# Optimization experiments

Hardware: AMD Instinct MI355X
Metric: run time of the kernel (lower is better)

Reference implementation:

```python
import jax, jax.numpy as jnp
import numpy as np
import math

NHEADS = 4


def _mab(Q, K, qw, qb, kw, kb, vw, vb, ow, ob, mask):
    """MAB2 from tripletformer: multi-head attention (head split via cat(split,0)),
    softmax scale uses sqrt(FULL dim_V), masked_fill(mask==0, -1e10), residual on
    the projected Q, then O + relu(fc_o(O))."""
    dv = qw.shape[1]
    dh = dv // NHEADS
    B, Nq, _ = Q.shape
    Nk = K.shape[1]
    Qh = (Q @ qw + qb).reshape(B, Nq, NHEADS, dh).transpose(0, 2, 1, 3)  # B,h,Nq,dh
    Kh = (K @ kw + kb).reshape(B, Nk, NHEADS, dh).transpose(0, 2, 1, 3)
    Vh = (K @ vw + vb).reshape(B, Nk, NHEADS, dh).transpose(0, 2, 1, 3)
    att = jnp.einsum('bhqd,bhkd->bhqk', Qh, Kh) * (1.0 / math.sqrt(dv))
    att = jnp.where(mask, att, jnp.asarray(-1e10, att.dtype))
    A = jax.nn.softmax(att, axis=-1)
    Oh = Qh + jnp.einsum('bhqk,bhkd->bhqd', A, Vh)
    O = Oh.transpose(0, 2, 1, 3).reshape(B, Nq, dv)
    return O + jax.nn.relu(O @ ow + ob)


def _forward(context_x, value, mask, obs_len, iff_w, iff_b, ind_points,
             q0w, q0b, k0w, k0b, v0w, v0b, o0w, o0b,
             q1w, q1b, k1w, k1b, v1w, v1b, o1w, o1b):
    B, L = context_x.shape
    D = value.shape[-1]
    mflat = mask.reshape(B, L * D)
    # stable stream compaction: observed entries first, original (time-major,
    # channel-minor) order preserved; truncate to static obs_len
    order = jnp.argsort(-mflat, axis=-1, stable=True)[:, :obs_len]  # (B, N)
    T = jnp.broadcast_to(context_x[:, :, None], (B, L, D)).reshape(B, L * D)
    C = jnp.broadcast_to(jnp.arange(D, dtype=jnp.int32), (B, L, D)).reshape(B, L * D)
    U = value.reshape(B, L * D)
    take = lambda a: jnp.take_along_axis(a, order, axis=-1)
    T_, U_, mk_ = take(T), take(U), take(mflat)
    Ch = jax.nn.one_hot(take(C), D, dtype=value.dtype)  # one_hot(num_classes=dim-2)
    X = jnp.concatenate([Ch, T_[..., None], U_[..., None]], axis=-1) * mk_[..., None]
    Y = jax.nn.relu(X @ iff_w + iff_b) * mk_[..., None]
    key_valid = mk_ > 0                        # (B, N)
    mask1 = key_valid[:, None, None, :]        # mab0: mask padded keys
    mask2 = key_valid[:, None, :, None]        # mab1: mask padded query rows
    Z = Y
    n_layers = ind_points.shape[0]
    for i in range(n_layers):
        I = jnp.broadcast_to(ind_points[i], (B,) + ind_points[i].shape)
        H = _mab(I, Z, q0w[i], q0b[i], k0w[i], k0b[i], v0w[i], v0b[i], o0w[i], o0b[i], mask1)
        Zn = _mab(Z, H, q1w[i], q1b[i], k1w[i], k1b[i], v1w[i], v1b[i], o1w[i], o1b[i], mask2)
        Z = Zn * mk_[..., None] + Z
    return Z, mk_[..., None]


def setup_inputs() -> dict:
    B, L, D, OBS, DK, M, NL = 16, 512, 41, 4096, 128, 128, 3
    key = jax.random.key(0)
    ks = jax.random.split(key, 16)
    context_x = jnp.sort(jax.random.uniform(ks[0], (B, L), dtype=jnp.float32), axis=-1)
    value = jax.random.normal(ks[1], (B, L, D), dtype=jnp.float32)
    # exactly OBS observed entries per batch row -> static packed length
    r = jax.random.uniform(ks[2], (B, L * D))
    kth = jnp.sort(r, axis=-1)[:, OBS]
    mask = (r < kth[:, None]).astype(jnp.float32).reshape(B, L, D)

    def w(k, shape, fan):
        return jax.random.normal(k, shape, dtype=jnp.float32) / math.sqrt(fan)

    inp = dict(
        context_x=context_x, value=value, mask=mask, obs_len=OBS,
        iff_w=w(ks[3], (D + 2, DK), D + 2), iff_b=jnp.zeros((DK,), jnp.float32),
        ind_points=w(ks[4], (NL, M, DK), DK),
    )
    for j, n in enumerate(['q0', 'k0', 'v0', 'o0', 'q1', 'k1', 'v1', 'o1']):
        inp[n + 'w'] = w(ks[5 + j], (NL, DK, DK), DK)
        inp[n + 'b'] = jnp.zeros((NL, DK), jnp.float32)
    return inp


def reference(context_x, value, mask, obs_len, iff_w, iff_b, ind_points,
              q0w, q0b, k0w, k0b, v0w, v0b, o0w, o0b,
              q1w, q1b, k1w, k1b, v1w, v1b, o1w, o1b):
    return _forward(context_x, value, mask, obs_len, iff_w, iff_b, ind_points,
                    q0w, q0b, k0w, k0b, v0w, v0b, o0w, o0b,
                    q1w, q1b, k1w, k1b, v1w, v1b, o1w, o1b)
```

## Files before the change

kernel.cpp:

```cpp
#include <hip/hip_runtime.h>
#include <math.h>

#define NBATCH 16
#define SEQL   512
#define DIM    41
#define LDFLAT (SEQL*DIM)
#define OBS    4096
#define DK     128
#define NH     4
#define DH     32

typedef short bf16x8 __attribute__((ext_vector_type(8)));
typedef short short8v __attribute__((ext_vector_type(8)));
typedef float floatx4 __attribute__((ext_vector_type(4)));

__device__ __forceinline__ short f2bf(float f) {
  union { float f; unsigned u; } v;
  v.f = f;
  unsigned r = (v.u + 0x7fffu + ((v.u >> 16) & 1u)) >> 16;
  return (short)r;
}
__device__ __forceinline__ float bf2f(short s) {
  union { unsigned u; float f; } v;
  v.u = ((unsigned)(unsigned short)s) << 16;
  return v.f;
}

__device__ __forceinline__ void stage_w(short* Wl, const short* __restrict__ Wt,
                                        int tid) {
#pragma unroll
  for (int i = tid * 8; i < 128 * 128; i += 2048)
    *(int4*)&Wl[(i >> 7) * 136 + (i & 127)] = *(const int4*)&Wt[i];
}
__device__ __forceinline__ void load_af(const short* Xl, int wv, int lm,
                                        int quad, bf16x8 af[4]) {
#pragma unroll
  for (int kc = 0; kc < 4; kc++)
    af[kc] = *(bf16x8*)&Xl[(wv * 16 + lm) * 136 + kc * 32 + quad * 8];
}
__device__ __forceinline__ void gemm8(const short* Wl, const bf16x8 af[4],
                                      int lm, int quad, floatx4 acc[8]) {
#pragma unroll
  for (int nt = 0; nt < 8; nt++) acc[nt] = (floatx4){0.f, 0.f, 0.f, 0.f};
#pragma unroll
  for (int kc = 0; kc < 4; kc++) {
    bf16x8 a = af[kc];
#pragma unroll
    for (int nt = 0; nt < 8; nt++) {
      bf16x8 b = *(bf16x8*)&Wl[(nt * 16 + lm) * 136 + kc * 32 + quad * 8];
      acc[nt] = __builtin_amdgcn_mfma_f32_16x16x32_bf16(a, b, acc[nt], 0, 0, 0);
    }
  }
}
__device__ __forceinline__ void store_sl(short* Sl, const floatx4 acc[8],
                                         const float* __restrict__ bias,
                                         int wv, int lm, int quad) {
#pragma unroll
  for (int nt = 0; nt < 8; nt++) {
    int col = nt * 16 + lm;
    float bn = bias[col];
#pragma unroll
    for (int r = 0; r < 4; r++)
      Sl[(wv * 16 + quad * 4 + r) * 136 + col] = f2bf(acc[nt][r] + bn);
  }
}
__device__ __forceinline__ void write_hs(const short* Sl,
                                         short* __restrict__ out, int rb,
                                         int nshift, int tid) {
  int rr = tid >> 2, hh = tid & 3;
  int r = rb + rr;
  int bb = r >> nshift, nn = r & ((1 << nshift) - 1);
  size_t o = (((size_t)(bb * NH + hh) << nshift) + nn) * 32;
#pragma unroll
  for (int j = 0; j < 4; j++)
    *(int4*)&out[o + j * 8] = *(int4*)&Sl[rr * 136 + hh * 32 + j * 8];
}

__global__ __launch_bounds__(1024) void prep_build_kernel(
    const float* __restrict__ q0w, const float* __restrict__ k0w,
    const float* __restrict__ v0w, const float* __restrict__ o0w,
    const float* __restrict__ q1w, const float* __restrict__ k1w,
    const float* __restrict__ v1w, const float* __restrict__ o1w,
    short* __restrict__ Wt,
    const float* __restrict__ mask, int* __restrict__ order,
    float* __restrict__ mk_out, float* __restrict__ mk_out2) {
  __shared__ float Tl[128 * 132];
  __shared__ int wsums[16];
  __shared__ int s_total_ones;
  __shared__ int s_chunk_ones;
  __shared__ int s_ones_base;
  __shared__ int s_zeros_base;
  int tid = threadIdx.x;

  if (blockIdx.x < 24) {
    int id = blockIdx.x, l = id >> 3, wi = id & 7;
    const float* s;
    switch (wi) {
      case 0: s = q0w; break; case 1: s = k0w; break;
      case 2: s = v0w; break; case 3: s = o0w; break;
      case 4: s = q1w; break; case 5: s = k1w; break;
      case 6: s = v1w; break; default: s = o1w; break;
    }
    s += (size_t)l * 16384;
    for (int i = tid * 4; i < 16384; i += 4096) {
      int k = i >> 7, n = i & 127;
      float4 x = *(const float4*)&s[i];
      Tl[k * 132 + n + 0] = x.x; Tl[k * 132 + n + 1] = x.y;
      Tl[k * 132 + n + 2] = x.z; Tl[k * 132 + n + 3] = x.w;
    }
    __syncthreads();
    short* dst = Wt + (size_t)id * 16384;
    int n = tid >> 3, k0 = (tid & 7) * 16;
    for (int jc = 0; jc < 2; jc++) {
      short8v t;
#pragma unroll
      for (int j = 0; j < 8; j++) t[j] = f2bf(Tl[(k0 + jc * 8 + j) * 132 + n]);
      *(short8v*)&dst[n * 128 + k0 + jc * 8] = t;
    }
    return;
  }

  int b = blockIdx.x - 24;
  const float* m = mask + (size_t)b * LDFLAT;
  int lane = tid & 63, w = tid >> 6;

  int cnt = 0;
  for (int j = tid; j < LDFLAT; j += 1024) cnt += (m[j] > 0.f) ? 1 : 0;
  for (int off = 32; off > 0; off >>= 1) cnt += __shfl_xor(cnt, off);
  if (lane == 0) wsums[w] = cnt;
  __syncthreads();
  if (tid == 0) {
    int t = 0;
    for (int i = 0; i < 16; i++) t += wsums[i];
    s_total_ones = t; s_ones_base = 0; s_zeros_base = 0;
  }
  __syncthreads();
  int total_ones = s_total_ones;

  for (int c0 = 0; c0 < LDFLAT; c0 += 1024) {
    __syncthreads();
    int j = c0 + tid;
    bool valid = (j < LDFLAT);
    float mv = valid ? m[j] : 0.f;
    int one = (valid && mv > 0.f) ? 1 : 0;
    int v = one;
    for (int off = 1; off < 64; off <<= 1) {
      int t = __shfl_up(v, (unsigned)off);
      if (lane >= off) v += t;
    }
    if (lane == 63) wsums[w] = v;
    __syncthreads();
    if (tid == 0) {
      int run = 0;
      for (int i = 0; i < 16; i++) { int t = wsums[i]; wsums[i] = run; run += t; }
      s_chunk_ones = run;
    }
    __syncthreads();
    int ones_before = (v - one) + wsums[w];
    int ob = s_ones_base, zb = s_zeros_base, chunk_ones = s_chunk_ones;
    int rem = LDFLAT - c0;
    int chunk_valid = rem < 1024 ? rem : 1024;
    int valid_before = tid < rem ? tid : rem;
    if (valid) {
      int pos = one ? (ob + ones_before)
                    : (total_ones + zb + (valid_before - ones_before));
      if (pos < OBS) {
        order[b * OBS + pos] = j;
        mk_out[b * OBS + pos] = mv;
        mk_out2[b * OBS + pos] = mv;
      }
    }
    __syncthreads();
    if (tid == 0) {
      s_ones_base = ob + chunk_ones;
      s_zeros_base = zb + (chunk_valid - chunk_ones);
    }
  }
}

__global__ __launch_bounds__(256) void fusedA_kernel(
    const int* __restrict__ order, const float* __restrict__ mk_g,
    const float* __restrict__ cx, const float* __restrict__ value,
    const float* __restrict__ iff_w, const float* __restrict__ iff_b,
    float* __restrict__ Z,
    const short* __restrict__ Wk, const float* __restrict__ kbias,
    short* __restrict__ Kb,
    const short* __restrict__ Wv, const float* __restrict__ vbias,
    short* __restrict__ Vb,
    const short* __restrict__ Wq, const float* __restrict__ qbias,
    short* __restrict__ Qb,
    const float* __restrict__ indp, const short* __restrict__ WtAll,
    const float* __restrict__ q0b_all, short* __restrict__ qh_b) {
  __shared__ __align__(16) short Xl[64 * 136];
  __shared__ __align__(16) short Wl[128 * 136];
  __shared__ int   rdd[64];
  __shared__ float rdt[64], rdu[64], rdm[64];
  int tid = threadIdx.x;
  int wv = tid >> 6, lane = tid & 63, lm = lane & 15, quad = lane >> 4;

  if (blockIdx.x >= 1024) {
    int id = blockIdx.x - 1024;
    int l = id >> 1, rbq = (id & 1) * 64;
    const float* X = indp + (size_t)l * 16384 + (size_t)rbq * 128;
    const short* W = WtAll + (size_t)(l * 8) * 16384;
    const float* bias = q0b_all + (size_t)l * 128;
    short* out = qh_b + (size_t)l * 16384;
    for (int i = tid * 4; i < 64 * 128; i += 1024) {
      int rr = i >> 7, c = i & 127;
      float4 x = *(const float4*)&X[i];
      *(short4*)&Xl[rr * 136 + c] =
          make_short4(f2bf(x.x), f2bf(x.y), f2bf(x.z), f2bf(x.w));
    }
    stage_w(Wl, W, tid);
    __syncthreads();
    bf16x8 af[4];
    load_af(Xl, wv, lm, quad, af);
    floatx4 acc[8];
    gemm8(Wl, af, lm, quad, acc);
    store_sl(Xl, acc, bias, wv, lm, quad);
    write_hs(Xl, out, rbq, 7, tid);
    return;
  }

  int rb = blockIdx.x * 64;
  if (tid < 64) {
    int idx = rb + tid;
    int b = idx >> 12;
    int j = order[idx];
    int l = j / DIM;
    rdd[tid] = j - l * DIM;
    rdt[tid] = cx[b * SEQL + l];
    rdu[tid] = value[(size_t)b * LDFLAT + j];
    rdm[tid] = mk_g[idx];
  }
  stage_w(Wl, Wk, tid);
  __syncthreads();
  for (int i = tid * 4; i < 64 * 128; i += 1024) {
    int rr = i >> 7, k = i & 127;
    float4 w0 = *(const float4*)&iff_w[rdd[rr] * DK + k];
    float4 w1 = *(const float4*)&iff_w[41 * DK + k];
    float4 w2 = *(const float4*)&iff_w[42 * DK + k];
    float4 b4 = *(const float4*)&iff_b[k];
    float t = rdt[rr], u = rdu[rr], mkv = rdm[rr];
    float4 z;
    z.x = fmaxf(w0.x + t * w1.x + u * w2.x + b4.x, 0.f) * mkv;
    z.y = fmaxf(w0.y + t * w1.y + u * w2.y + b4.y, 0.f) * mkv;
    z.z = fmaxf(w0.z + t * w1.z + u * w2.z + b4.z, 0.f) * mkv;
    z.w = fmaxf(w0.w + t * w1.w + u * w2.w + b4.w, 0.f) * mkv;
    *(float4*)&Z[(size_t)(rb + rr) * DK + k] = z;
    *(short4*)&Xl[rr * 136 + k] =
        make_short4(f2bf(z.x), f2bf(z.y), f2bf(z.z), f2bf(z.w));
  }
  __syncthreads();
  bf16x8 af[4];
  load_af(Xl, wv, lm, quad, af);
  floatx4 acc[8];
  gemm8(Wl, af, lm, quad, acc);
  store_sl(Xl, acc, kbias, wv, lm, quad);
  write_hs(Xl, Kb, rb, 12, tid);
  __syncthreads();
  stage_w(Wl, Wv, tid);
  __syncthreads();
  gemm8(Wl, af, lm, quad, acc);
  store_sl(Xl, acc, vbias, wv, lm, quad);
  write_hs(Xl, Vb, rb, 12, tid);
  __syncthreads();
  stage_w(Wl, Wq, tid);
  __syncthreads();
  gemm8(Wl, af, lm, quad, acc);
  store_sl(Xl, acc, qbias, wv, lm, quad);
  write_hs(Xl, Qb, rb, 12, tid);
}

__global__ __launch_bounds__(256) void attn1_kernel(
    const short* __restrict__ Qh,
    const short* __restrict__ Kh, const short* __restrict__ Vh,
    const float* __restrict__ mk,
    float* __restrict__ Opart, float* __restrict__ mpart,
    float* __restrict__ lpart) {
  __shared__ __align__(16) short Ql[128 * 40];
  __shared__ __align__(16) short Kc[64 * 40];
  __shared__ __align__(16) short Vtc[32 * 72];
  __shared__ __align__(16) short Pl[128 * 72];
  __shared__ float mkc[64];
  int bh = blockIdx.x;
  int b = bh >> 2, h = bh & 3;
  int ks = blockIdx.y;
  int tid = threadIdx.x;
  int wv = tid >> 6, lane = tid & 63, lm = lane & 15, quad = lane >> 4;

  const short* qbg = Qh + (size_t)h * 128 * 32;
  for (int i = tid * 8; i < 128 * 32; i += 2048) {
    int r = i >> 5, c = i & 31;
    *(int4*)&Ql[r * 40 + c] = *(const int4*)&qbg[i];
  }
  __syncthreads();
  bf16x8 aq[2];
  aq[0] = *(bf16x8*)&Ql[(wv * 32 + lm) * 40 + quad * 8];
  aq[1] = *(bf16x8*)&Ql[(wv * 32 + 16 + lm) * 40 + quad * 8];

  float m_i[2][4], l_i[2][4];
  floatx4 oacc[2][2];
#pragma unroll
  for (int mt = 0; mt < 2; mt++) {
#pragma unroll
    for (int r = 0; r < 4; r++) { m_i[mt][r] = -1e30f; l_i[mt][r] = 0.f; }
    oacc[mt][0] = (floatx4){0.f, 0.f, 0.f, 0.f};
    oacc[mt][1] = (floatx4){0.f, 0.f, 0.f, 0.f};
  }
  const float scale = 0.08838834764831845f;
  const short* kbase = Kh + ((size_t)bh * OBS + ks * 512) * 32;
  const short* vbase = Vh + ((size_t)bh * OBS + ks * 512) * 32;
  const float* mkb = mk + (size_t)b * OBS + ks * 512;

  for (int ch = 0; ch < 8; ch++) {
    __syncthreads();
    {
      int i = tid * 8;
      int r = i >> 5, c = i & 31;
      *(int4*)&Kc[r * 40 + c] = *(const int4*)&kbase[ch * 2048 + i];
      int4 vv4 = *(const int4*)&vbase[ch * 2048 + i];
      short* vv = (short*)&vv4;
#pragma unroll
      for (int j = 0; j < 8; j++) Vtc[(c + j) * 72 + r] = vv[j];
    }
    if (tid < 64) mkc[tid] = mkb[ch * 64 + tid];
    __syncthreads();

    floatx4 sf[2][4];
#pragma unroll
    for (int nt = 0; nt < 4; nt++) {
      bf16x8 bfrag = *(bf16x8*)&Kc[(nt * 16 + lm) * 40 + quad * 8];
      floatx4 z = {0.f, 0.f, 0.f, 0.f};
      sf[0][nt] = __builtin_amdgcn_mfma_f32_16x16x32_bf16(aq[0], bfrag, z, 0, 0, 0);
      sf[1][nt] = __builtin_amdgcn_mfma_f32_16x16x32_bf16(aq[1], bfrag, z, 0, 0, 0);
    }
#pragma unroll
    for (int nt = 0; nt < 4; nt++) {
      float mkv = mkc[nt * 16 + lm];
      bool ok = mkv > 0.f;
#pragma unroll
      for (int mt = 0; mt < 2; mt++)
#pragma unroll
        for (int r = 0; r < 4; r++)
          sf[mt][nt][r] = ok ? sf[mt][nt][r] * scale : -1e10f;
    }
#pragma unroll
    for (int mt = 0; mt < 2; mt++) {
#pragma unroll
      for (int r = 0; r < 4; r++) {
        float mx = fmaxf(fmaxf(sf[mt][0][r], sf[mt][1][r]),
                         fmaxf(sf[mt][2][r], sf[mt][3][r]));
        mx = fmaxf(mx, __shfl_xor(mx, 1));
        mx = fmaxf(mx, __shfl_xor(mx, 2));
        mx = fmaxf(mx, __shfl_xor(mx, 4));
        mx = fmaxf(mx, __shfl_xor(mx, 8));
        float mn = fmaxf(m_i[mt][r], mx);
        float al = __expf(m_i[mt][r] - mn);
        float ps = 0.f;
#pragma unroll
        for (int nt = 0; nt < 4; nt++) {
          float p = __expf(sf[mt][nt][r] - mn);
          sf[mt][nt][r] = p;
          ps += p;
        }
        ps += __shfl_xor(ps, 1);
        ps += __shfl_xor(ps, 2);
        ps += __shfl_xor(ps, 4);
        ps += __shfl_xor(ps, 8);
        l_i[mt][r] = l_i[mt][r] * al + ps;
        m_i[mt][r] = mn;
        oacc[mt][0] *= al;
        oacc[mt][1] *= al;
      }
    }
#pragma unroll
    for (int mt = 0; mt < 2; mt++)
#pragma unroll
      for (int nt = 0; nt < 4; nt++)
#pragma unroll
        for (int r = 0; r < 4; r++)
          Pl[(wv * 32 + mt * 16 + quad * 4 + r) * 72 + nt * 16 + lm] =
              f2bf(sf[mt][nt][r]);
#pragma unroll
    for (int kc = 0; kc < 2; kc++) {
      bf16x8 vf0 = *(bf16x8*)&Vtc[lm * 72 + kc * 32 + quad * 8];
      bf16x8 vf1 = *(bf16x8*)&Vtc[(16 + lm) * 72 + kc * 32 + quad * 8];
#pragma unroll
      for (int mt = 0; mt < 2; mt++) {
        bf16x8 pf = *(bf16x8*)&Pl[(wv * 32 + mt * 16 + lm) * 72 + kc * 32 + quad * 8];
        oacc[mt][0] = __builtin_amdgcn_mfma_f32_16x16x32_bf16(pf, vf0, oacc[mt][0], 0, 0, 0);
        oacc[mt][1] = __builtin_amdgcn_mfma_f32_16x16x32_bf16(pf, vf1, oacc[mt][1], 0, 0, 0);
      }
    }
  }
  float* ob = Opart + (size_t)(ks * 64 + bh) * 128 * 32;
#pragma unroll
  for (int mt = 0; mt < 2; mt++) {
#pragma unroll
    for (int r = 0; r < 4; r++) {
      int row = wv * 32 + mt * 16 + quad * 4 + r;
      ob[(size_t)row * 32 + lm] = oacc[mt][0][r];
      ob[(size_t)row * 32 + 16 + lm] = oacc[mt][1][r];
      if (lm == 0) {
        mpart[(size_t)(ks * 64 + bh) * 128 + row] = m_i[mt][r];
        lpart[(size_t)(ks * 64 + bh) * 128 + row] = l_i[mt][r];
      }
    }
  }
}

__global__ __launch_bounds__(256) void fusedB_kernel(
    const float* __restrict__ Opart, const float* __restrict__ mpart,
    const float* __restrict__ lpart, const short* __restrict__ qh,
    const short* __restrict__ Wo, const float* __restrict__ obias,
    const short* __restrict__ Wk, const float* __restrict__ kbias,
    const short* __restrict__ Wv, const float* __restrict__ vbias,
    short* __restrict__ khb, short* __restrict__ vhb) {
  __shared__ __align__(16) short Xl[64 * 136];
  __shared__ __align__(16) short Wl[128 * 136];
  int tid = threadIdx.x;
  int rb = blockIdx.x * 64;
  int b = rb >> 7, n0 = rb & 127;
  {
    int rr = tid >> 2, hh = tid & 3;
    int n = n0 + rr;
    int bh = b * 4 + hh;
    float mv[8], lv[8], m = -1e30f;
#pragma unroll
    for (int s = 0; s < 8; s++) {
      mv[s] = mpart[(size_t)(s * 64 + bh) * 128 + n];
      lv[s] = lpart[(size_t)(s * 64 + bh) * 128 + n];
      m = fmaxf(m, mv[s]);
    }
    float l = 0.f;
    float oa[32];
#pragma unroll
    for (int d = 0; d < 32; d++) oa[d] = 0.f;
#pragma unroll
    for (int s = 0; s < 8; s++) {
      float w = __expf(mv[s] - m);
      l += lv[s] * w;
      const float* op = &Opart[((size_t)(s * 64 + bh) * 128 + n) * 32];
#pragma unroll
      for (int d4 = 0; d4 < 8; d4++) {
        float4 v = *(const float4*)&op[d4 * 4];
        oa[d4 * 4 + 0] += v.x * w; oa[d4 * 4 + 1] += v.y * w;
        oa[d4 * 4 + 2] += v.z * w; oa[d4 * 4 + 3] += v.w * w;
      }
    }
    float li = 1.f / l;
    const short* qp = &qh[((size_t)hh * 128 + n) * 32];
#pragma unroll
    for (int d = 0; d < 32; d++)
      Xl[rr * 136 + hh * 32 + d] = f2bf(bf2f(qp[d]) + oa[d] * li);
  }
  stage_w(Wl, Wo, tid);
  __syncthreads();
  int wv = tid >> 6, lane = tid & 63, lm = lane & 15, quad = lane >> 4;
  bf16x8 af[4];
  load_af(Xl, wv, lm, quad, af);
  floatx4 acc[8];
  gemm8(Wl, af, lm, quad, acc);
#pragma unroll
  for (int nt = 0; nt < 8; nt++) {
    int col = nt * 16 + lm;
    float bn = obias[col];
#pragma unroll
    for (int r = 0; r < 4; r++) {
      int row = wv * 16 + quad * 4 + r;
      float ov = bf2f(Xl[row * 136 + col]);
      Xl[row * 136 + col] = f2bf(ov + fmaxf(acc[nt][r] + bn, 0.f));
    }
  }
  load_af(Xl, wv, lm, quad, af);
  __syncthreads();
  stage_w(Wl, Wk, tid);
  __syncthreads();
  gemm8(Wl, af, lm, quad, acc);
  store_sl(Xl, acc, kbias, wv, lm, quad);
  write_hs(Xl, khb, rb, 7, tid);
  __syncthreads();
  stage_w(Wl, Wv, tid);
  __syncthreads();
  gemm8(Wl, af, lm, quad, acc);
  store_sl(Xl, acc, vbias, wv, lm, quad);
  write_hs(Xl, vhb, rb, 7, tid);
}

__global__ __launch_bounds__(256) void attn2_kernel(
    const short* __restrict__ Qh, const short* __restrict__ Kh,
    const short* __restrict__ Vh, short* __restrict__ O) {
  __shared__ __align__(16) short Kl[128 * 40];
  __shared__ __align__(16) short Vt[32 * 136];
  __shared__ __align__(16) short Ql[64 * 40];
  __shared__ __align__(16) short Pl[64 * 136];
  int bh = blockIdx.x;
  int b = bh >> 2, h = bh & 3;
  int q0 = blockIdx.y * 64;
  int tid = threadIdx.x;
  int wv = tid >> 6, lane = tid & 63, lm = lane & 15, quad = lane >> 4;
  const short* kb = Kh + (size_t)bh * 128 * 32;
  const short* vb = Vh + (size_t)bh * 128 * 32;
  const short* qb = Qh + ((size_t)bh * OBS + q0) * 32;

  for (int i = tid * 8; i < 128 * 32; i += 2048) {
    int r = i >> 5, c = i & 31;
    *(int4*)&Kl[r * 40 + c] = *(const int4*)&kb[i];
  }
  for (int i = tid * 8; i < 64 * 32; i += 2048) {
    int r = i >> 5, c = i & 31;
    *(int4*)&Ql[r * 40 + c] = *(const int4*)&qb[i];
  }
  for (int i = tid * 8; i < 128 * 32; i += 2048) {
    int r = i >> 5, c = i & 31;
    int4 vv4 = *(const int4*)&vb[i];
    short* vv = (short*)&vv4;
#pragma unroll
    for (int j = 0; j < 8; j++) Vt[(c + j) * 136 + r] = vv[j];
  }
  __syncthreads();

  const float scale = 0.08838834764831845f;
  bf16x8 afrag = *(bf16x8*)&Ql[(wv * 16 + lm) * 40 + quad * 8];
  floatx4 sf[8];
#pragma unroll
  for (int nt = 0; nt < 8; nt++) {
    bf16x8 bfrag = *(bf16x8*)&Kl[(nt * 16 + lm) * 40 + quad * 8];
    floatx4 z = {0.f, 0.f, 0.f, 0.f};
    sf[nt] = __builtin_amdgcn_mfma_f32_16x16x32_bf16(afrag, bfrag, z, 0, 0, 0);
  }
#pragma unroll
  for (int nt = 0; nt < 8; nt++) sf[nt] *= scale;
  float linv[4];
#pragma unroll
  for (int r = 0; r < 4; r++) {
    float mx = sf[0][r];
#pragma unroll
    for (int nt = 1; nt < 8; nt++) mx = fmaxf(mx, sf[nt][r]);
    mx = fmaxf(mx, __shfl_xor(mx, 1));
    mx = fmaxf(mx, __shfl_xor(mx, 2));
    mx = fmaxf(mx, __shfl_xor(mx, 4));
    mx = fmaxf(mx, __shfl_xor(mx, 8));
    float sum = 0.f;
#pragma unroll
    for (int nt = 0; nt < 8; nt++) {
      float p = __expf(sf[nt][r] - mx);
      sf[nt][r] = p;
      sum += p;
    }
    sum += __shfl_xor(sum, 1);
    sum += __shfl_xor(sum, 2);
    sum += __shfl_xor(sum, 4);
    sum += __shfl_xor(sum, 8);
    linv[r] = 1.f / sum;
  }
#pragma unroll
  for (int nt = 0; nt < 8; nt++)
#pragma unroll
    for (int r = 0; r < 4; r++)
      Pl[(wv * 16 + quad * 4 + r) * 136 + nt * 16 + lm] = f2bf(sf[nt][r]);

  floatx4 oacc[2] = {{0.f, 0.f, 0.f, 0.f}, {0.f, 0.f, 0.f, 0.f}};
#pragma unroll
  for (int kc = 0; kc < 4; kc++) {
    bf16x8 pf = *(bf16x8*)&Pl[(wv * 16 + lm) * 136 + kc * 32 + quad * 8];
#pragma unroll
    for (int nt2 = 0; nt2 < 2; nt2++) {
      bf16x8 vf = *(bf16x8*)&Vt[(nt2 * 16 + lm) * 136 + kc * 32 + quad * 8];
      oacc[nt2] = __builtin_amdgcn_mfma_f32_16x16x32_bf16(pf, vf, oacc[nt2], 0, 0, 0);
    }
  }
  short* Ol = Pl;
#pragma unroll
  for (int nt2 = 0; nt2 < 2; nt2++) {
#pragma unroll
    for (int r = 0; r < 4; r++) {
      int qrow = wv * 16 + quad * 4 + r;
      float q = bf2f(Ql[qrow * 40 + nt2 * 16 + lm]);
      Ol[qrow * 136 + nt2 * 16 + lm] = f2bf(q + oacc[nt2][r] * linv[r]);
    }
  }
  int rr = tid >> 2, seg = tid & 3;
  size_t o = ((size_t)b * OBS + q0 + rr) * 128 + h * 32 + seg * 8;
  *(int4*)&O[o] = *(int4*)&Ol[rr * 136 + seg * 8];
}

__global__ __launch_bounds__(256) void fusedC_kernel(
    const short* __restrict__ Ob, const short* __restrict__ Wo,
    const float* __restrict__ obias, const float* __restrict__ mk,
    const float* __restrict__ Zin, float* __restrict__ Zout,
    const short* __restrict__ Wk, const float* __restrict__ kbias,
    short* __restrict__ Kb,
    const short* __restrict__ Wv, const float* __restrict__ vbias,
    short* __restrict__ Vb,
    const short* __restrict__ Wq, const float* __restrict__ qbias,
    short* __restrict__ Qb) {
  __shared__ __align__(16) short Xl[64 * 136];
  __shared__ __align__(16) short Wl[128 * 136];
  int tid = threadIdx.x;
  int rb = blockIdx.x * 64;
  int wv = tid >> 6, lane = tid & 63, lm = lane & 15, quad = lane >> 4;
  for (int i = tid * 8; i < 64 * 128; i += 2048) {
    int rr = i >> 7, c = i & 127;
    *(int4*)&Xl[rr * 136 + c] = *(const int4*)&Ob[(size_t)(rb + rr) * 136 - (size_t)(rb + rr) * 8 + c];
  }
  stage_w(Wl, Wo, tid);
  __syncthreads();
  bf16x8 af[4];
  load_af(Xl, wv, lm, quad, af);
  floatx4 acc[8];
  gemm8(Wl, af, lm, quad, acc);
  __syncthreads();
  float* Fl = (float*)Wl;
#pragma unroll
  for (int nt = 0; nt < 8; nt++) {
    int col = nt * 16 + lm;
    float bn = obias[col];
#pragma unroll
    for (int r = 0; r < 4; r++) {
      int row = wv * 16 + quad * 4 + r;
      int gr = rb + row;
      float ov = bf2f(Xl[row * 136 + col]);
      float f = ov + fmaxf(acc[nt][r] + bn, 0.f);
      Fl[row * 132 + col] = Zin[(size_t)gr * 128 + col] + f * mk[gr];
    }
  }
  {
    int rr = tid >> 2, seg = tid & 3;
    int gr = rb + rr;
#pragma unroll
    for (int j = 0; j < 8; j++) {
      float4 f = *(float4*)&Fl[rr * 132 + seg * 32 + j * 4];
      *(float4*)&Zout[(size_t)gr * 128 + seg * 32 + j * 4] = f;
      if (Wk)
        *(short4*)&Xl[rr * 136 + seg * 32 + j * 4] =
            make_short4(f2bf(f.x), f2bf(f.y), f2bf(f.z), f2bf(f.w));
    }
  }
  if (Wk == nullptr) return;
  load_af(Xl, wv, lm, quad, af);
  __syncthreads();
  stage_w(Wl, Wk, tid);
  __syncthreads();
  gemm8(Wl, af, lm, quad, acc);
  store_sl(Xl, acc, kbias, wv, lm, quad);
  write_hs(Xl, Kb, rb, 12, tid);
  __syncthreads();
  stage_w(Wl, Wv, tid);
  __syncthreads();
  gemm8(Wl, af, lm, quad, acc);
  store_sl(Xl, acc, vbias, wv, lm, quad);
  write_hs(Xl, Vb, rb, 12, tid);
  __syncthreads();
  stage_w(Wl, Wq, tid);
  __syncthreads();
  gemm8(Wl, af, lm, quad, acc);
  store_sl(Xl, acc, qbias, wv, lm, quad);
  write_hs(Xl, Qb, rb, 12, tid);
}

extern "C" void kernel_launch(void* const* d_in, const int* in_sizes, int n_in,
                              void* d_out, int out_size, void* d_ws,
                              size_t ws_size, hipStream_t stream) {
  const float* cx    = (const float*)d_in[0];
  const float* value = (const float*)d_in[1];
  const float* mask  = (const float*)d_in[2];
  const float* iff_w = (const float*)d_in[4];
  const float* iff_b = (const float*)d_in[5];
  const float* indp  = (const float*)d_in[6];
  const float* q0w = (const float*)d_in[7];  const float* q0b = (const float*)d_in[8];
  const float* k0w = (const float*)d_in[9];  const float* k0b = (const float*)d_in[10];
  const float* v0w = (const float*)d_in[11]; const float* v0b = (const float*)d_in[12];
  const float* o0w = (const float*)d_in[13]; const float* o0b = (const float*)d_in[14];
  const float* q1w = (const float*)d_in[15]; const float* q1b = (const float*)d_in[16];
  const float* k1w = (const float*)d_in[17]; const float* k1b = (const float*)d_in[18];
  const float* v1w = (const float*)d_in[19]; const float* v1b = (const float*)d_in[20];
  const float* o1w = (const float*)d_in[21]; const float* o1b = (const float*)d_in[22];

  char* ws = (char*)d_ws;
  short* Wt    = (short*)ws;  ws += (size_t)24 * 16384 * 2;
  int*   order = (int*)ws;    ws += (size_t)NBATCH * OBS * 4;
  float* mk_g  = (float*)ws;  ws += (size_t)NBATCH * OBS * 4;
  float* Z     = (float*)ws;  ws += (size_t)NBATCH * OBS * DK * 4;
  short* Qb    = (short*)ws;  ws += (size_t)NBATCH * OBS * DK * 2;
  short* Kb    = (short*)ws;  ws += (size_t)NBATCH * OBS * DK * 2;
  short* Vb    = (short*)ws;  ws += (size_t)NBATCH * OBS * DK * 2;
  short* Ob    = (short*)ws;  ws += (size_t)NBATCH * OBS * DK * 2;
  short* qh_b  = (short*)ws;  ws += (size_t)3 * 128 * DK * 2;
  short* khb   = (short*)ws;  ws += (size_t)NBATCH * NH * 128 * DH * 2;
  short* vhb   = (short*)ws;  ws += (size_t)NBATCH * NH * 128 * DH * 2;
  float* Opart = (float*)ws;  ws += (size_t)8 * 64 * 128 * 32 * 4;
  float* mpart = (float*)ws;  ws += (size_t)8 * 64 * 128 * 4;
  float* lpart = (float*)ws;  ws += (size_t)8 * 64 * 128 * 4;

  float* outZ  = (float*)d_out;
  float* outMk = outZ + (size_t)NBATCH * OBS * DK;

  prep_build_kernel<<<40, 1024, 0, stream>>>(q0w, k0w, v0w, o0w, q1w, k1w,
                                             v1w, o1w, Wt, mask, order, mk_g,
                                             outMk);

  const short* W[3][8];
  for (int l = 0; l < 3; l++)
    for (int wi = 0; wi < 8; wi++) W[l][wi] = Wt + (size_t)(l * 8 + wi) * 16384;

  fusedA_kernel<<<1030, 256, 0, stream>>>(
      order, mk_g, cx, value, iff_w, iff_b, Z,
      W[0][1], k0b, Kb, W[0][2], v0b, Vb, W[0][4], q1b, Qb,
      indp, Wt, q0b, qh_b);

  for (int l = 0; l < 3; l++) {
    attn1_kernel<<<dim3(64, 8), 256, 0, stream>>>(
        qh_b + (size_t)l * 16384, Kb, Vb, mk_g, Opart, mpart, lpart);
    fusedB_kernel<<<32, 256, 0, stream>>>(
        Opart, mpart, lpart, qh_b + (size_t)l * 16384,
        W[l][3], o0b + (size_t)l * 128,
        W[l][5], k1b + (size_t)l * 128,
        W[l][6], v1b + (size_t)l * 128, khb, vhb);
    attn2_kernel<<<dim3(64, 64), 256, 0, stream>>>(Qb, khb, vhb, Ob);
    if (l < 2) {
      fusedC_kernel<<<1024, 256, 0, stream>>>(
          Ob, W[l][7], o1b + (size_t)l * 128, mk_g, Z, Z,
          W[l + 1][1], k0b + (size_t)(l + 1) * 128, Kb,
          W[l + 1][2], v0b + (size_t)(l + 1) * 128, Vb,
          W[l + 1][4], q1b + (size_t)(l + 1) * 128, Qb);
    } else {
      fusedC_kernel<<<1024, 256, 0, stream>>>(
          Ob, W[l][7], o1b + (size_t)l * 128, mk_g, Z, outZ,
          nullptr, nullptr, nullptr, nullptr, nullptr, nullptr,
          nullptr, nullptr, nullptr);
    }
  }
}
```

Baseline: 513.2 us.

## Read GEMM weight fragments directly from global memory instead of staging in LDS

The fused projection kernels (A, B, C) no longer copy each 128x128 bf16 weight matrix into a shared-memory tile before the MFMA loop. Each lane now loads its B-fragment straight from global memory, which relies on L1/L2 caching of the small weight matrices. This removes the weight LDS buffer and most block-wide barriers, and launch bounds now ask for four blocks per CU to raise occupancy. Per-row input staging is also reorganised so each wave fills only the rows it later reads. The trade-off is strided, partly uncoalesced global fragment loads in place of LDS reads, and some removed barriers may now let waves overwrite the shared scratch tile while other waves still read it.

```diff
diff --git a/kernel.cpp b/kernel.cpp
--- a/kernel.cpp
+++ b/kernel.cpp
@@ -26,31 +26,27 @@
   return v.f;
 }
 
-__device__ __forceinline__ void stage_w(short* Wl, const short* __restrict__ Wt,
-                                        int tid) {
-#pragma unroll
-  for (int i = tid * 8; i < 128 * 128; i += 2048)
-    *(int4*)&Wl[(i >> 7) * 136 + (i & 127)] = *(const int4*)&Wt[i];
+
+__device__ __forceinline__ void gemm8_g(const short* __restrict__ Wg,
+                                        const bf16x8 af[4], int lm, int quad,
+                                        floatx4 acc[8]) {
+#pragma unroll
+  for (int nt = 0; nt < 8; nt++) acc[nt] = (floatx4){0.f, 0.f, 0.f, 0.f};
+#pragma unroll
+  for (int kc = 0; kc < 4; kc++) {
+    bf16x8 a = af[kc];
+#pragma unroll
+    for (int nt = 0; nt < 8; nt++) {
+      bf16x8 b = *(const bf16x8*)&Wg[(size_t)(nt * 16 + lm) * 128 + kc * 32 + quad * 8];
+      acc[nt] = __builtin_amdgcn_mfma_f32_16x16x32_bf16(a, b, acc[nt], 0, 0, 0);
+    }
+  }
 }
 __device__ __forceinline__ void load_af(const short* Xl, int wv, int lm,
                                         int quad, bf16x8 af[4]) {
 #pragma unroll
   for (int kc = 0; kc < 4; kc++)
     af[kc] = *(bf16x8*)&Xl[(wv * 16 + lm) * 136 + kc * 32 + quad * 8];
-}
-__device__ __forceinline__ void gemm8(const short* Wl, const bf16x8 af[4],
-                                      int lm, int quad, floatx4 acc[8]) {
-#pragma unroll
-  for (int nt = 0; nt < 8; nt++) acc[nt] = (floatx4){0.f, 0.f, 0.f, 0.f};
-#pragma unroll
-  for (int kc = 0; kc < 4; kc++) {
-    bf16x8 a = af[kc];
-#pragma unroll
-    for (int nt = 0; nt < 8; nt++) {
-      bf16x8 b = *(bf16x8*)&Wl[(nt * 16 + lm) * 136 + kc * 32 + quad * 8];
-      acc[nt] = __builtin_amdgcn_mfma_f32_16x16x32_bf16(a, b, acc[nt], 0, 0, 0);
-    }
-  }
 }
 __device__ __forceinline__ void store_sl(short* Sl, const floatx4 acc[8],
                                          const float* __restrict__ bias,
@@ -178,7 +174,7 @@
   }
 }
 
-__global__ __launch_bounds__(256) void fusedA_kernel(
+__global__ __launch_bounds__(256, 4) void fusedA_kernel(
     const int* __restrict__ order, const float* __restrict__ mk_g,
     const float* __restrict__ cx, const float* __restrict__ value,
     const float* __restrict__ iff_w, const float* __restrict__ iff_b,
@@ -192,11 +188,10 @@
     const float* __restrict__ indp, const short* __restrict__ WtAll,
     const float* __restrict__ q0b_all, short* __restrict__ qh_b) {
   __shared__ __align__(16) short Xl[64 * 136];
-  __shared__ __align__(16) short Wl[128 * 136];
-  __shared__ int   rdd[64];
-  __shared__ float rdt[64], rdu[64], rdm[64];
   int tid = threadIdx.x;
   int wv = tid >> 6, lane = tid & 63, lm = lane & 15, quad = lane >> 4;
+  int r_l = lane >> 2, seg = lane & 3;
+  int lrow = wv * 16 + r_l;
 
   if (blockIdx.x >= 1024) {
     int id = blockIdx.x - 1024;
@@ -205,69 +200,57 @@
     const short* W = WtAll + (size_t)(l * 8) * 16384;
     const float* bias = q0b_all + (size_t)l * 128;
     short* out = qh_b + (size_t)l * 16384;
-    for (int i = tid * 4; i < 64 * 128; i += 1024) {
-      int rr = i >> 7, c = i & 127;
-      float4 x = *(const float4*)&X[i];
-      *(short4*)&Xl[rr * 136 + c] =
+    const float* Xr = X + (size_t)lrow * 128;
+#pragma unroll
+    for (int jj = 0; jj < 8; jj++) {
+      int col = seg * 32 + jj * 4;
+      float4 x = *(const float4*)&Xr[col];
+      *(short4*)&Xl[lrow * 136 + col] =
           make_short4(f2bf(x.x), f2bf(x.y), f2bf(x.z), f2bf(x.w));
     }
-    stage_w(Wl, W, tid);
-    __syncthreads();
     bf16x8 af[4];
     load_af(Xl, wv, lm, quad, af);
     floatx4 acc[8];
-    gemm8(Wl, af, lm, quad, acc);
+    gemm8_g(W, af, lm, quad, acc);
     store_sl(Xl, acc, bias, wv, lm, quad);
     write_hs(Xl, out, rbq, 7, tid);
     return;
   }
 
   int rb = blockIdx.x * 64;
-  if (tid < 64) {
-    int idx = rb + tid;
-    int b = idx >> 12;
-    int j = order[idx];
-    int l = j / DIM;
-    rdd[tid] = j - l * DIM;
-    rdt[tid] = cx[b * SEQL + l];
-    rdu[tid] = value[(size_t)b * LDFLAT + j];
-    rdm[tid] = mk_g[idx];
-  }
-  stage_w(Wl, Wk, tid);
-  __syncthreads();
-  for (int i = tid * 4; i < 64 * 128; i += 1024) {
-    int rr = i >> 7, k = i & 127;
-    float4 w0 = *(const float4*)&iff_w[rdd[rr] * DK + k];
-    float4 w1 = *(const float4*)&iff_w[41 * DK + k];
-    float4 w2 = *(const float4*)&iff_w[42 * DK + k];
-    float4 b4 = *(const float4*)&iff_b[k];
-    float t = rdt[rr], u = rdu[rr], mkv = rdm[rr];
+  int grow = rb + lrow;
+  int bb = grow >> 12;
+  int j = order[grow];
+  int l = j / DIM, d = j - l * DIM;
+  float t = cx[bb * SEQL + l];
+  float u = value[(size_t)bb * LDFLAT + j];
+  float mkv = mk_g[grow];
+#pragma unroll
+  for (int jj = 0; jj < 8; jj++) {
+    int col = seg * 32 + jj * 4;
+    float4 w0 = *(const float4*)&iff_w[d * DK + col];
+    float4 w1 = *(const float4*)&iff_w[41 * DK + col];
+    float4 w2 = *(const float4*)&iff_w[42 * DK + col];
+    float4 b4 = *(const float4*)&iff_b[col];
     float4 z;
     z.x = fmaxf(w0.x + t * w1.x + u * w2.x + b4.x, 0.f) * mkv;
     z.y = fmaxf(w0.y + t * w1.y + u * w2.y + b4.y, 0.f) * mkv;
     z.z = fmaxf(w0.z + t * w1.z + u * w2.z + b4.z, 0.f) * mkv;
     z.w = fmaxf(w0.w + t * w1.w + u * w2.w + b4.w, 0.f) * mkv;
-    *(float4*)&Z[(size_t)(rb + rr) * DK + k] = z;
-    *(short4*)&Xl[rr * 136 + k] =
+    *(float4*)&Z[(size_t)grow * DK + col] = z;
+    *(short4*)&Xl[lrow * 136 + col] =
         make_short4(f2bf(z.x), f2bf(z.y), f2bf(z.z), f2bf(z.w));
   }
-  __syncthreads();
   bf16x8 af[4];
   load_af(Xl, wv, lm, quad, af);
   floatx4 acc[8];
-  gemm8(Wl, af, lm, quad, acc);
+  gemm8_g(Wk, af, lm, quad, acc);
   store_sl(Xl, acc, kbias, wv, lm, quad);
   write_hs(Xl, Kb, rb, 12, tid);
-  __syncthreads();
-  stage_w(Wl, Wv, tid);
-  __syncthreads();
-  gemm8(Wl, af, lm, quad, acc);
+  gemm8_g(Wv, af, lm, quad, acc);
   store_sl(Xl, acc, vbias, wv, lm, quad);
   write_hs(Xl, Vb, rb, 12, tid);
-  __syncthreads();
-  stage_w(Wl, Wq, tid);
-  __syncthreads();
-  gemm8(Wl, af, lm, quad, acc);
+  gemm8_g(Wq, af, lm, quad, acc);
   store_sl(Xl, acc, qbias, wv, lm, quad);
   write_hs(Xl, Qb, rb, 12, tid);
 }
@@ -410,7 +393,7 @@
   }
 }
 
-__global__ __launch_bounds__(256) void fusedB_kernel(
+__global__ __launch_bounds__(256, 4) void fusedB_kernel(
     const float* __restrict__ Opart, const float* __restrict__ mpart,
     const float* __restrict__ lpart, const short* __restrict__ qh,
     const short* __restrict__ Wo, const float* __restrict__ obias,
@@ -418,10 +401,10 @@
     const short* __restrict__ Wv, const float* __restrict__ vbias,
     short* __restrict__ khb, short* __restrict__ vhb) {
   __shared__ __align__(16) short Xl[64 * 136];
-  __shared__ __align__(16) short Wl[128 * 136];
   int tid = threadIdx.x;
   int rb = blockIdx.x * 64;
   int b = rb >> 7, n0 = rb & 127;
+  int wv = tid >> 6, lane = tid & 63, lm = lane & 15, quad = lane >> 4;
   {
     int rr = tid >> 2, hh = tid & 3;
     int n = n0 + rr;
@@ -455,13 +438,10 @@
     for (int d = 0; d < 32; d++)
       Xl[rr * 136 + hh * 32 + d] = f2bf(bf2f(qp[d]) + oa[d] * li);
   }
-  stage_w(Wl, Wo, tid);
-  __syncthreads();
-  int wv = tid >> 6, lane = tid & 63, lm = lane & 15, quad = lane >> 4;
   bf16x8 af[4];
   load_af(Xl, wv, lm, quad, af);
   floatx4 acc[8];
-  gemm8(Wl, af, lm, quad, acc);
+  gemm8_g(Wo, af, lm, quad, acc);
 #pragma unroll
   for (int nt = 0; nt < 8; nt++) {
     int col = nt * 16 + lm;
@@ -474,16 +454,10 @@
     }
   }
   load_af(Xl, wv, lm, quad, af);
-  __syncthreads();
-  stage_w(Wl, Wk, tid);
-  __syncthreads();
-  gemm8(Wl, af, lm, quad, acc);
+  gemm8_g(Wk, af, lm, quad, acc);
   store_sl(Xl, acc, kbias, wv, lm, quad);
   write_hs(Xl, khb, rb, 7, tid);
-  __syncthreads();
-  stage_w(Wl, Wv, tid);
-  __syncthreads();
-  gemm8(Wl, af, lm, quad, acc);
+  gemm8_g(Wv, af, lm, quad, acc);
   store_sl(Xl, acc, vbias, wv, lm, quad);
   write_hs(Xl, vhb, rb, 7, tid);
 }
@@ -586,7 +560,7 @@
   *(int4*)&O[o] = *(int4*)&Ol[rr * 136 + seg * 8];
 }
 
-__global__ __launch_bounds__(256) void fusedC_kernel(
+__global__ __launch_bounds__(256, 4) void fusedC_kernel(
     const short* __restrict__ Ob, const short* __restrict__ Wo,
     const float* __restrict__ obias, const float* __restrict__ mk,
     const float* __restrict__ Zin, float* __restrict__ Zout,
@@ -597,65 +571,47 @@
     const short* __restrict__ Wq, const float* __restrict__ qbias,
     short* __restrict__ Qb) {
   __shared__ __align__(16) short Xl[64 * 136];
-  __shared__ __align__(16) short Wl[128 * 136];
   int tid = threadIdx.x;
   int rb = blockIdx.x * 64;
   int wv = tid >> 6, lane = tid & 63, lm = lane & 15, quad = lane >> 4;
-  for (int i = tid * 8; i < 64 * 128; i += 2048) {
-    int rr = i >> 7, c = i & 127;
-    *(int4*)&Xl[rr * 136 + c] = *(const int4*)&Ob[(size_t)(rb + rr) * 136 - (size_t)(rb + rr) * 8 + c];
-  }
-  stage_w(Wl, Wo, tid);
-  __syncthreads();
+
   bf16x8 af[4];
-  load_af(Xl, wv, lm, quad, af);
+  {
+    const short* arow = Ob + (size_t)(rb + wv * 16 + lm) * 128;
+#pragma unroll
+    for (int kc = 0; kc < 4; kc++)
+      af[kc] = *(const bf16x8*)&arow[kc * 32 + quad * 8];
+  }
   floatx4 acc[8];
-  gemm8(Wl, af, lm, quad, acc);
-  __syncthreads();
-  float* Fl = (float*)Wl;
+  gemm8_g(Wo, af, lm, quad, acc);
+
+  int row0 = wv * 16 + quad * 4;
+  float mkv[4];
+#pragma unroll
+  for (int r = 0; r < 4; r++) mkv[r] = mk[rb + row0 + r];
 #pragma unroll
   for (int nt = 0; nt < 8; nt++) {
     int col = nt * 16 + lm;
     float bn = obias[col];
 #pragma unroll
     for (int r = 0; r < 4; r++) {
-      int row = wv * 16 + quad * 4 + r;
-      int gr = rb + row;
-      float ov = bf2f(Xl[row * 136 + col]);
+      size_t g = (size_t)(rb + row0 + r) * 128 + col;
+      float ov = bf2f(Ob[g]);
       float f = ov + fmaxf(acc[nt][r] + bn, 0.f);
-      Fl[row * 132 + col] = Zin[(size_t)gr * 128 + col] + f * mk[gr];
-    }
-  }
-  {
-    int rr = tid >> 2, seg = tid & 3;
-    int gr = rb + rr;
-#pragma unroll
-    for (int j = 0; j < 8; j++) {
-      float4 f = *(float4*)&Fl[rr * 132 + seg * 32 + j * 4];
-      *(float4*)&Zout[(size_t)gr * 128 + seg * 32 + j * 4] = f;
-      if (Wk)
-        *(short4*)&Xl[rr * 136 + seg * 32 + j * 4] =
-            make_short4(f2bf(f.x), f2bf(f.y), f2bf(f.z), f2bf(f.w));
+      float zv = Zin[g] + f * mkv[r];
+      Zout[g] = zv;
+      Xl[(row0 + r) * 136 + col] = f2bf(zv);
     }
   }
   if (Wk == nullptr) return;
   load_af(Xl, wv, lm, quad, af);
-  __syncthreads();
-  stage_w(Wl, Wk, tid);
-  __syncthreads();
-  gemm8(Wl, af, lm, quad, acc);
+  gemm8_g(Wk, af, lm, quad, acc);
   store_sl(Xl, acc, kbias, wv, lm, quad);
   write_hs(Xl, Kb, rb, 12, tid);
-  __syncthreads();
-  stage_w(Wl, Wv, tid);
-  __syncthreads();
-  gemm8(Wl, af, lm, quad, acc);
+  gemm8_g(Wv, af, lm, quad, acc);
   store_sl(Xl, acc, vbias, wv, lm, quad);
   write_hs(Xl, Vb, rb, 12, tid);
-  __syncthreads();
-  stage_w(Wl, Wq, tid);
-  __syncthreads();
-  gemm8(Wl, af, lm, quad, acc);
+  gemm8_g(Wq, af, lm, quad, acc);
   store_sl(Xl, acc, qbias, wv, lm, quad);
   write_hs(Xl, Qb, rb, 12, tid);
 }
```

New measurement: 625.6 us. 21.9% more time.
